# Optimization experiments

Hardware: AMD Instinct MI355X
Metric: run time of the kernel (lower is better)

The kernel has to match this reference:

```python
import jax, jax.numpy as jnp
import numpy as np

ANCHOR_PX = (32, 64, 96, 128)
FIELD = 16.0
POOL, TILES = 2, 3
TAU, NMS_IOU = 0.5, 0.3
MAX_DET = 512
HF, WF, DF = 128, 128, 512
HIDDEN = 1024


def _create_anchors():
    # anchors centered on the field grid, rows ordered (i, j, k): x,y = upper-left, w=h=size
    ii, jj, kk = np.meshgrid(np.arange(HF), np.arange(WF), np.arange(len(ANCHOR_PX)), indexing='ij')
    sz = np.asarray(ANCHOR_PX, np.float32)[kk]
    x = jj * FIELD + FIELD / 2 - sz / 2
    y = ii * FIELD + FIELD / 2 - sz / 2
    return np.stack([x.ravel(), y.ravel(), sz.ravel(), sz.ravel()], axis=1).astype(np.float32)


def setup_inputs() -> dict:
    key = jax.random.key(0)
    ks = jax.random.split(key, 8)
    return {
        'features': jax.random.normal(ks[0], (HF, WF, DF), jnp.float32),
        'rpn_obj': jax.random.normal(ks[1], (HF, WF, 2 * len(ANCHOR_PX)), jnp.float32),
        'rpn_reg': 0.1 * jax.random.normal(ks[2], (HF, WF, 4 * len(ANCHOR_PX)), jnp.float32),
        'anchors': jnp.asarray(_create_anchors()),
        'W1': 0.02 * jax.random.normal(ks[3], (TILES * TILES * DF, HIDDEN), jnp.float32),
        'b1': jnp.zeros((HIDDEN,), jnp.float32),
        'W2': 0.02 * jax.random.normal(ks[4], (HIDDEN, HIDDEN), jnp.float32),
        'b2': jnp.zeros((HIDDEN,), jnp.float32),
        'W3': 0.02 * jax.random.normal(ks[5], (HIDDEN, 4), jnp.float32),
        'b3': jnp.zeros((4,), jnp.float32),
    }


def _map_outputs(output, anchors):
    # faithful port of map_outputs: 3D RPN tensor -> per-anchor rows via gather
    K = len(ANCHOR_PX)
    ap = jnp.asarray(ANCHOR_PX, jnp.float32)
    idx = jnp.argmax(anchors[:, 3:4] == ap[None, :], axis=1).astype(jnp.int32)
    px = ((anchors[:, 0] + anchors[:, 2] / 2) / FIELD).astype(jnp.int32)
    py = ((anchors[:, 1] + anchors[:, 3] / 2) / FIELD).astype(jnp.int32)
    H, W, D = output.shape
    reshaped = output.reshape(H, W, K, D // K)
    return reshaped[py, px, idx]  # (Na, D//K)


def _unparameterize(reg, anchors):
    acx = anchors[:, 0] + anchors[:, 2] / 2
    acy = anchors[:, 1] + anchors[:, 3] / 2
    cx = acx + reg[:, 0] * anchors[:, 2]
    cy = acy + reg[:, 1] * anchors[:, 3]
    w = anchors[:, 2] * jnp.exp(reg[:, 2])
    h = anchors[:, 3] * jnp.exp(reg[:, 3])
    return jnp.stack([cx - w / 2, cy - h / 2, w, h], axis=1)


def _iou_matrix(boxes):
    x1, y1 = boxes[:, 0], boxes[:, 1]
    x2, y2 = x1 + boxes[:, 2], y1 + boxes[:, 3]
    ix = jnp.maximum(0.0, jnp.minimum(x2[:, None], x2[None, :]) - jnp.maximum(x1[:, None], x1[None, :]))
    iy = jnp.maximum(0.0, jnp.minimum(y2[:, None], y2[None, :]) - jnp.maximum(y1[:, None], y1[None, :]))
    inter = ix * iy
    area = boxes[:, 2] * boxes[:, 3]
    return inter / (area[:, None] + area[None, :] - inter + 1e-8)


def _nms_keep(iou, valid, thr):
    # greedy NMS on score-sorted boxes: sequential scan over rows
    n = valid.shape[0]
    rng = jnp.arange(n)
    def step(keep, i):
        suppressed = jnp.any((iou[i] > thr) & keep & (rng < i))
        k = valid[i] & jnp.logical_not(suppressed)
        return keep.at[i].set(k), k
    keep, _ = jax.lax.scan(step, jnp.zeros((n,), bool), rng)
    return keep


def _roialign(features, boxes):
    # pool x pool bilinear samples per tile, tiles x tiles tiles per box, max-pooled per tile
    M = boxes.shape[0]
    T = TILES * POOL
    t = (jnp.arange(T, dtype=jnp.float32) + 0.5) / T
    fx = (boxes[:, 0:1] + t[None, :] * boxes[:, 2:3]) / FIELD - 0.5  # (M, T)
    fy = (boxes[:, 1:2] + t[None, :] * boxes[:, 3:4]) / FIELD - 0.5
    def grid(c, n):
        c = jnp.clip(c, 0.0, n - 1.0)
        c0 = jnp.floor(c).astype(jnp.int32)
        c1 = jnp.minimum(c0 + 1, n - 1)
        return c0, c1, c - c0
    x0, x1, wx = grid(fx, WF)
    y0, y1, wy = grid(fy, HF)
    def g(yi, xi):
        return features[yi[:, :, None], xi[:, None, :]]  # (M, T, T, D)
    wy0, wy1 = (1 - wy)[:, :, None, None], wy[:, :, None, None]
    wx0, wx1 = (1 - wx)[:, None, :, None], wx[:, None, :, None]
    val = g(y0, x0) * wy0 * wx0 + g(y0, x1) * wy0 * wx1 + g(y1, x0) * wy1 * wx0 + g(y1, x1) * wy1 * wx1
    val = val.reshape(M, TILES, POOL, TILES, POOL, DF)
    return jnp.max(val, axis=(2, 4))  # (M, TILES, TILES, D)


def reference(features, rpn_obj, rpn_reg, anchors, W1, b1, W2, b2, W3, b3):
    obj = _map_outputs(rpn_obj, anchors)            # (Na, 2)
    reg = _map_outputs(rpn_reg, anchors)            # (Na, 4)
    scores = jax.nn.softmax(obj, axis=1)[:, 1]      # objectness
    boxes = _unparameterize(reg, anchors)           # proposals (Na, 4)
    # threshold + top-k (fixed-shape surrogate for boolean_mask)
    masked = jnp.where(scores > TAU, scores, -jnp.inf)
    top_scores, top_idx = jax.lax.top_k(masked, MAX_DET)
    valid = jnp.isfinite(top_scores)
    sel = boxes[top_idx]                            # (MAX_DET, 4)
    keep = _nms_keep(_iou_matrix(sel), valid, NMS_IOU)
    # roialign + fast-rcnn refinement head
    pooled = _roialign(features, sel).reshape(MAX_DET, -1)
    h = jax.nn.relu(pooled @ W1 + b1)
    h = jax.nn.relu(h @ W2 + b2)
    deltas = h @ W3 + b3
    refined = _unparameterize(deltas, sel)
    sc = jnp.where(valid, top_scores, 0.0)
    out = jnp.concatenate([refined, sc[:, None]], axis=1)
    return out * keep[:, None].astype(out.dtype)    # (MAX_DET, 5)
```

## Files before the change

kernel.cpp:

```cpp
#include <hip/hip_runtime.h>
#include <math.h>

#define HFD 128
#define WFD 128
#define DFD 512
#define KA  4
#define NA  (HFD*WFD*KA)
#define MAXD 512
#define HID 1024
#define FIN 4608
#define CMAX 2048
#define NBUCK 1025
#define BINCAP 64
#define TAUF 0.5f
#define NMS_THR 0.3f
#define SPLITK 8

typedef __bf16 bf16x8 __attribute__((ext_vector_type(8)));
typedef float  floatx4 __attribute__((ext_vector_type(4)));

__device__ __forceinline__ unsigned short f2bf(float x) {
    unsigned u = __float_as_uint(x);
    unsigned r = (u + 0x7FFFu + ((u >> 16) & 1u)) >> 16;
    return (unsigned short)r;
}

__global__ __launch_bounds__(256)
void front_kernel(const float* __restrict__ rpn_obj,
                  unsigned* __restrict__ hist,
                  unsigned long long* __restrict__ bins,
                  const float* __restrict__ W1,
                  unsigned short* __restrict__ W1t,
                  const float* __restrict__ W2,
                  unsigned short* __restrict__ W2t) {
    __shared__ float tile[32][33];
    int b = blockIdx.x;
    if (b < 256) {
        int n = b * 256 + threadIdx.x;
        float2 o = ((const float2*)rpn_obj)[n];
        float m  = fmaxf(o.x, o.y);
        float e0 = expf(o.x - m), e1 = expf(o.y - m);
        float s  = e1 / (e0 + e1);
        if (s > TAUF) {
            unsigned bits = __float_as_uint(s);
            unsigned bk = (bits - 0x3F000000u) >> 13;
            unsigned slot = atomicAdd(&hist[bk], 1u);
            if (slot < BINCAP)
                bins[bk * BINCAP + slot] =
                    ((unsigned long long)bits << 32) |
                    (unsigned long long)(~(unsigned)n);
        }
        return;
    }
    b -= 256;
    const float* W; unsigned short* Wt; int K, N;
    if (b < (FIN / 32) * (HID / 32)) { W = W1; Wt = W1t; K = FIN; N = HID; }
    else { b -= (FIN / 32) * (HID / 32); W = W2; Wt = W2t; K = HID; N = HID; }
    int bn = (b & (N / 32 - 1)) * 32;
    int bk = (b / (N / 32)) * 32;
    int tx = threadIdx.x & 31, ty = threadIdx.x >> 5;
#pragma unroll
    for (int r = 0; r < 32; r += 8)
        tile[ty + r][tx] = W[(long)(bk + ty + r) * N + bn + tx];
    __syncthreads();
#pragma unroll
    for (int r = 0; r < 32; r += 8)
        Wt[(long)(bn + ty + r) * K + bk + tx] = f2bf(tile[tx][ty + r]);
}

__global__ __launch_bounds__(1024)
void tgs_kernel(const unsigned* __restrict__ hist,
                const unsigned long long* __restrict__ bins,
                const float* __restrict__ rpn_reg,
                const float* __restrict__ anchors,
                float* __restrict__ sel,
                float* __restrict__ top_score,
                unsigned* __restrict__ valid_g) {
    __shared__ unsigned long long keys[CMAX];
    __shared__ unsigned Hs[NBUCK];
    __shared__ unsigned Ssc[1024];
    __shared__ unsigned cntS;
    __shared__ unsigned thrS;

    int tid = threadIdx.x;
    int wave = tid >> 6, lane = tid & 63;

    if (tid == 0) cntS = 0u;
    for (int i = tid; i < NBUCK; i += 1024) Hs[i] = hist[i];
    __syncthreads();
    unsigned sv = Hs[tid + 1];
    Ssc[tid] = sv;
    __syncthreads();
    for (int d = 1; d < 1024; d <<= 1) {
        unsigned add = (tid + d < 1024) ? Ssc[tid + d] : 0u;
        __syncthreads();
        Ssc[tid] += add;
        __syncthreads();
    }
    if (tid == 0 && Ssc[0] < MAXD) thrS = 0u;
    {
        unsigned Scur = Ssc[tid];
        unsigned Snxt = (tid == 1023) ? 0u : Ssc[tid + 1];
        if (Scur >= MAXD && Snxt < MAXD) thrS = (unsigned)(tid + 1);
    }
    __syncthreads();
    unsigned thr = thrS;

    for (int b = (int)thr + wave; b < NBUCK; b += 16) {
        unsigned c = Hs[b]; if (c > BINCAP) c = BINCAP;
        unsigned base = 0;
        if (lane == 0 && c > 0) base = atomicAdd(&cntS, c);
        base = __shfl(base, 0);
        if (c > 0 && lane < c && base + lane < CMAX)
            keys[base + lane] = bins[(long)b * BINCAP + lane];
    }
    __syncthreads();
    unsigned cnt = cntS; if (cnt > CMAX) cnt = CMAX;
    int SN = (cnt <= 1024) ? 1024 : CMAX;
    for (int i = tid; i < SN; i += 1024)
        if (i >= (int)cnt) keys[i] = 0ULL;
    __syncthreads();

    for (int k = 2; k <= SN; k <<= 1) {
        for (int j = k >> 1; j > 0; j >>= 1) {
            for (int i = tid; i < SN; i += 1024) {
                int ixj = i ^ j;
                if (ixj > i) {
                    unsigned long long a = keys[i], b = keys[ixj];
                    bool up = ((i & k) == 0);
                    if ((a < b) == up) { keys[i] = b; keys[ixj] = a; }
                }
            }
            __syncthreads();
        }
    }

    if (tid < MAXD) {
        unsigned long long e = keys[tid];
        unsigned sbits = (unsigned)(e >> 32);
        bool v = (sbits != 0u);
        unsigned idx = v ? (unsigned)(~(unsigned)e) : 0u;
        int cell = idx >> 2, kk = idx & 3;
        float4 rg = *(const float4*)&rpn_reg[cell * 16 + 4 * kk];
        float4 an = *(const float4*)&anchors[idx * 4];
        float acx = an.x + an.z * 0.5f;
        float acy = an.y + an.w * 0.5f;
        float cx = acx + rg.x * an.z;
        float cy = acy + rg.y * an.w;
        float w  = an.z * expf(rg.z);
        float h  = an.w * expf(rg.w);
        ((float4*)sel)[tid] = make_float4(cx - 0.5f * w, cy - 0.5f * h, w, h);
        top_score[tid] = v ? __uint_as_float(sbits) : 0.0f;
        valid_g[tid]   = v ? 1u : 0u;
    }
}

__global__ __launch_bounds__(512)
void iou_mask_kernel(const float* __restrict__ sel,
                     unsigned long long* __restrict__ mask) {
    int i = blockIdx.x;
    int j = threadIdx.x;
    float4 bi = ((const float4*)sel)[i];
    float4 bj = ((const float4*)sel)[j];
    float x2i = bi.x + bi.z, y2i = bi.y + bi.w;
    float x2j = bj.x + bj.z, y2j = bj.y + bj.w;
    float ai = bi.z * bi.w, aj = bj.z * bj.w;
    float ix = fmaxf(0.0f, fminf(x2i, x2j) - fmaxf(bi.x, bj.x));
    float iy = fmaxf(0.0f, fminf(y2i, y2j) - fmaxf(bi.y, bj.y));
    float inter = ix * iy;
    float iou = inter / (ai + aj - inter + 1e-8f);
    unsigned long long bal = __ballot(iou > NMS_THR);
    if ((j & 63) == 0) mask[i * 8 + (j >> 6)] = bal;
}

__global__ __launch_bounds__(64)
void nms_scan_kernel(const unsigned long long* __restrict__ mask,
                     const unsigned* __restrict__ valid,
                     unsigned* __restrict__ cidx,
                     unsigned* __restrict__ nkeep) {
    int lane = threadIdx.x;
    unsigned long long w[8][8];
#pragma unroll
    for (int g = 0; g < 8; ++g)
#pragma unroll
        for (int t = 0; t < 8; ++t)
            if (t <= g) w[g][t] = mask[(g * 64 + lane) * 8 + t];
    unsigned long long vb[8];
#pragma unroll
    for (int g = 0; g < 8; ++g)
        vb[g] = __ballot(valid[g * 64 + lane] != 0u);

    unsigned long long keepw[8];
#pragma unroll
    for (int g = 0; g < 8; ++g) {
        bool pre = false;
#pragma unroll
        for (int t = 0; t < 8; ++t)
            if (t < g) pre = pre || ((w[g][t] & keepw[t]) != 0ULL);
        unsigned long long alive = vb[g] & ~__ballot(pre);
        unsigned long long intra = w[g][g];
        unsigned long long kg = 0ULL;
        while (alive) {
            int b = __builtin_ctzll(alive);
            unsigned long long bit = 1ULL << b;
            kg |= bit;
            unsigned long long sup = __ballot((intra >> b) & 1ULL);
            alive &= ~(sup | bit);
        }
        keepw[g] = kg;
    }
    unsigned total = 0;
#pragma unroll
    for (int g = 0; g < 8; ++g) {
        unsigned long long kg = keepw[g];
        if ((kg >> lane) & 1ULL) {
            unsigned pos = total +
                (unsigned)__builtin_popcountll(kg & ((1ULL << lane) - 1ULL));
            cidx[pos] = (unsigned)(g * 64 + lane);
        }
        total += (unsigned)__builtin_popcountll(kg);
    }
    if (lane == 0) nkeep[0] = total;
}

__global__ __launch_bounds__(256)
void roialign_kernel(const float* __restrict__ feat,
                     const float* __restrict__ sel,
                     const unsigned* __restrict__ cidx,
                     const unsigned* __restrict__ nkeep,
                     unsigned short* __restrict__ pooled) {
    int m = blockIdx.x;
    if (m >= (int)nkeep[0]) return;
    int mrow = (int)cidx[m];
    int c = threadIdx.x;
    float4 b = ((const float4*)sel)[mrow];
    float bx = b.x, by = b.y, bw = b.z, bh = b.w;
    float vmax0[9], vmax1[9];
#pragma unroll
    for (int t = 0; t < 9; ++t) { vmax0[t] = -INFINITY; vmax1[t] = -INFINITY; }
#pragma unroll
    for (int p = 0; p < 6; ++p) {
        float fy = (by + ((float)p + 0.5f) / 6.0f * bh) / 16.0f - 0.5f;
        fy = fminf(fmaxf(fy, 0.0f), 127.0f);
        int y0 = (int)floorf(fy);
        int y1 = min(y0 + 1, 127);
        float wy = fy - (float)y0;
#pragma unroll
        for (int q = 0; q < 6; ++q) {
            float fx = (bx + ((float)q + 0.5f) / 6.0f * bw) / 16.0f - 0.5f;
            fx = fminf(fmaxf(fx, 0.0f), 127.0f);
            int x0 = (int)floorf(fx);
            int x1 = min(x0 + 1, 127);
            float wx = fx - (float)x0;
            const float* f00 = feat + (y0 * WFD + x0) * DFD;
            const float* f01 = feat + (y0 * WFD + x1) * DFD;
            const float* f10 = feat + (y1 * WFD + x0) * DFD;
            const float* f11 = feat + (y1 * WFD + x1) * DFD;
            float w00 = (1.0f - wy) * (1.0f - wx);
            float w01 = (1.0f - wy) * wx;
            float w10 = wy * (1.0f - wx);
            float w11 = wy * wx;
            int t = (p >> 1) * 3 + (q >> 1);
            float v0 = f00[c] * w00 + f01[c] * w01 + f10[c] * w10 + f11[c] * w11;
            float v1 = f00[c + 256] * w00 + f01[c + 256] * w01 +
                       f10[c + 256] * w10 + f11[c + 256] * w11;
            vmax0[t] = fmaxf(vmax0[t], v0);
            vmax1[t] = fmaxf(vmax1[t], v1);
        }
    }
#pragma unroll
    for (int t = 0; t < 9; ++t) {
        pooled[m * FIN + t * DFD + c] = f2bf(vmax0[t]);
        pooled[m * FIN + t * DFD + c + 256] = f2bf(vmax1[t]);
    }
}

#define LDSTRIDE 40
__global__ __launch_bounds__(256)
void mfma_gemm_kernel(const unsigned short* __restrict__ A,
                      const unsigned short* __restrict__ Bt,
                      float* __restrict__ Cpart,
                      const unsigned* __restrict__ nkeep,
                      int M, int N, int K) {
    int bm = blockIdx.y * 64;
    if (bm >= (int)nkeep[0]) return;
    __shared__ unsigned short As[64 * LDSTRIDE];
    __shared__ unsigned short Bs[64 * LDSTRIDE];
    int tid = threadIdx.x;
    int wave = tid >> 6, lane = tid & 63;
    int bn = blockIdx.x * 64;
    int KC = K / SPLITK;
    int ks = blockIdx.z * KC;

    floatx4 acc[4] = {};
    int lr = tid >> 2;
    int lk = (tid & 3) << 3;
    int frow = lane & 15, quad = lane >> 4;

    const unsigned short* Ap = A + (long)(bm + lr) * K + lk;
    const unsigned short* Bp = Bt + (long)(bn + lr) * K + lk;

    for (int k0 = ks; k0 < ks + KC; k0 += 32) {
        uint4 av = *(const uint4*)(Ap + k0);
        uint4 bv = *(const uint4*)(Bp + k0);
        *(uint4*)&As[lr * LDSTRIDE + lk] = av;
        *(uint4*)&Bs[lr * LDSTRIDE + lk] = bv;
        __syncthreads();
        bf16x8 af = *(const bf16x8*)&As[(wave * 16 + frow) * LDSTRIDE + quad * 8];
#pragma unroll
        for (int t = 0; t < 4; ++t) {
            bf16x8 bfv = *(const bf16x8*)&Bs[(t * 16 + frow) * LDSTRIDE + quad * 8];
            acc[t] = __builtin_amdgcn_mfma_f32_16x16x32_bf16(af, bfv, acc[t], 0, 0, 0);
        }
        __syncthreads();
    }

    float* Cp = Cpart + (long)blockIdx.z * M * N;
#pragma unroll
    for (int t = 0; t < 4; ++t) {
#pragma unroll
        for (int r = 0; r < 4; ++r) {
            int m = bm + wave * 16 + quad * 4 + r;
            int n = bn + t * 16 + frow;
            Cp[(long)m * N + n] = acc[t][r];
        }
    }
}

__global__ __launch_bounds__(256)
void reduce_bias_relu_kernel(const float* __restrict__ Cpart,
                             const float* __restrict__ bias,
                             unsigned short* __restrict__ out_bf,
                             const unsigned* __restrict__ nkeep,
                             int MN, int N) {
    int i4 = (blockIdx.x * blockDim.x + threadIdx.x) * 4;
    if (i4 >= MN) return;
    if ((unsigned)(i4 >> 10) >= nkeep[0]) return;
    float4 s = *(const float4*)&Cpart[i4];
#pragma unroll
    for (int z = 1; z < SPLITK; ++z) {
        float4 p = *(const float4*)&Cpart[(long)z * MN + i4];
        s.x += p.x; s.y += p.y; s.z += p.z; s.w += p.w;
    }
    int n = i4 & (N - 1);
    float4 bi = *(const float4*)&bias[n];
    s.x = fmaxf(s.x + bi.x, 0.0f);
    s.y = fmaxf(s.y + bi.y, 0.0f);
    s.z = fmaxf(s.z + bi.z, 0.0f);
    s.w = fmaxf(s.w + bi.w, 0.0f);
    uint2 o;
    o.x = (unsigned)f2bf(s.x) | ((unsigned)f2bf(s.y) << 16);
    o.y = (unsigned)f2bf(s.z) | ((unsigned)f2bf(s.w) << 16);
    *(uint2*)&out_bf[i4] = o;
}

__global__ __launch_bounds__(256)
void rowhead_kernel(const float* __restrict__ Cpart,
                    const float* __restrict__ b2,
                    const float* __restrict__ W3,
                    const float* __restrict__ b3,
                    const float* __restrict__ sel,
                    const float* __restrict__ top_score,
                    const unsigned* __restrict__ cidx,
                    const unsigned* __restrict__ nkeep,
                    float* __restrict__ out) {
    int p = blockIdx.x;
    if (p >= (int)nkeep[0]) return;
    __shared__ float red[4][4];
    int t = threadIdx.x;
    int wave = t >> 6, lane = t & 63;
    int c = t * 4;
    const int MN = MAXD * HID;
    float4 s = *(const float4*)&Cpart[(long)p * HID + c];
#pragma unroll
    for (int z = 1; z < SPLITK; ++z) {
        float4 q = *(const float4*)&Cpart[(long)z * MN + (long)p * HID + c];
        s.x += q.x; s.y += q.y; s.z += q.z; s.w += q.w;
    }
    float4 bi = *(const float4*)&b2[c];
    float h[4];
    h[0] = fmaxf(s.x + bi.x, 0.0f);
    h[1] = fmaxf(s.y + bi.y, 0.0f);
    h[2] = fmaxf(s.z + bi.z, 0.0f);
    h[3] = fmaxf(s.w + bi.w, 0.0f);
    float a0 = 0.f, a1 = 0.f, a2 = 0.f, a3 = 0.f;
#pragma unroll
    for (int i = 0; i < 4; ++i) {
        float4 w = *(const float4*)&W3[(c + i) * 4];
        a0 += h[i] * w.x; a1 += h[i] * w.y;
        a2 += h[i] * w.z; a3 += h[i] * w.w;
    }
#pragma unroll
    for (int off = 32; off > 0; off >>= 1) {
        a0 += __shfl_down(a0, off);
        a1 += __shfl_down(a1, off);
        a2 += __shfl_down(a2, off);
        a3 += __shfl_down(a3, off);
    }
    if (lane == 0) {
        red[wave][0] = a0; red[wave][1] = a1;
        red[wave][2] = a2; red[wave][3] = a3;
    }
    __syncthreads();
    if (t == 0) {
        int r = (int)cidx[p];
        float d0 = red[0][0] + red[1][0] + red[2][0] + red[3][0] + b3[0];
        float d1 = red[0][1] + red[1][1] + red[2][1] + red[3][1] + b3[1];
        float d2 = red[0][2] + red[1][2] + red[2][2] + red[3][2] + b3[2];
        float d3 = red[0][3] + red[1][3] + red[2][3] + red[3][3] + b3[3];
        float4 b = ((const float4*)sel)[r];
        float acx = b.x + 0.5f * b.z;
        float acy = b.y + 0.5f * b.w;
        float cx = acx + d0 * b.z;
        float cy = acy + d1 * b.w;
        float nw = b.z * expf(d2);
        float nh = b.w * expf(d3);
        out[r * 5 + 0] = cx - 0.5f * nw;
        out[r * 5 + 1] = cy - 0.5f * nh;
        out[r * 5 + 2] = nw;
        out[r * 5 + 3] = nh;
        out[r * 5 + 4] = top_score[r];
    }
}

extern "C" void kernel_launch(void* const* d_in, const int* in_sizes, int n_in,
                              void* d_out, int out_size, void* d_ws, size_t ws_size,
                              hipStream_t stream) {
    const float* features = (const float*)d_in[0];
    const float* rpn_obj  = (const float*)d_in[1];
    const float* rpn_reg  = (const float*)d_in[2];
    const float* anchors  = (const float*)d_in[3];
    const float* W1 = (const float*)d_in[4];
    const float* b1 = (const float*)d_in[5];
    const float* W2 = (const float*)d_in[6];
    const float* b2 = (const float*)d_in[7];
    const float* W3 = (const float*)d_in[8];
    const float* b3 = (const float*)d_in[9];
    float* out = (float*)d_out;

    char* ws = (char*)d_ws;
    size_t off = 0;
    auto alloc = [&](size_t bytes) {
        char* p = ws + off;
        off += (bytes + 255) & ~(size_t)255;
        return p;
    };
    unsigned* hist      = (unsigned*)alloc(NBUCK * sizeof(unsigned));
    unsigned long long* bins =
        (unsigned long long*)alloc((size_t)NBUCK * BINCAP * 8);
    float*    sel       = (float*)alloc(MAXD * 4 * sizeof(float));
    float*    top_score = (float*)alloc(MAXD * sizeof(float));
    unsigned* valid     = (unsigned*)alloc(MAXD * sizeof(unsigned));
    unsigned* cidx      = (unsigned*)alloc(MAXD * sizeof(unsigned));
    unsigned* nkeep     = (unsigned*)alloc(sizeof(unsigned));
    unsigned long long* mask = (unsigned long long*)alloc(MAXD * 8 * 8);
    unsigned short* pooled = (unsigned short*)alloc((size_t)MAXD * FIN * 2);
    unsigned short* W1t = (unsigned short*)alloc((size_t)FIN * HID * 2);
    unsigned short* W2t = (unsigned short*)alloc((size_t)HID * HID * 2);
    unsigned short* h1  = (unsigned short*)alloc((size_t)MAXD * HID * 2);
    float*    Cpart     = (float*)alloc((size_t)SPLITK * MAXD * HID * sizeof(float));
    (void)ws_size; (void)in_sizes; (void)n_in;

    hipMemsetAsync(hist, 0, NBUCK * sizeof(unsigned), stream);
    hipMemsetAsync(out, 0, (size_t)out_size * sizeof(float), stream);

    const int TBLOCKS = (FIN / 32) * (HID / 32) + (HID / 32) * (HID / 32);
    front_kernel<<<256 + TBLOCKS, 256, 0, stream>>>(rpn_obj, hist, bins,
                                                    W1, W1t, W2, W2t);
    tgs_kernel<<<1, 1024, 0, stream>>>(hist, bins, rpn_reg, anchors,
                                       sel, top_score, valid);
    iou_mask_kernel<<<MAXD, 512, 0, stream>>>(sel, mask);
    nms_scan_kernel<<<1, 64, 0, stream>>>(mask, valid, cidx, nkeep);
    roialign_kernel<<<MAXD, 256, 0, stream>>>(features, sel, cidx, nkeep,
                                              pooled);

    const int MN = MAXD * HID;
    mfma_gemm_kernel<<<dim3(HID / 64, MAXD / 64, SPLITK), 256, 0, stream>>>(
        pooled, W1t, Cpart, nkeep, MAXD, HID, FIN);
    reduce_bias_relu_kernel<<<MN / 4 / 256, 256, 0, stream>>>(
        Cpart, b1, h1, nkeep, MN, HID);
    mfma_gemm_kernel<<<dim3(HID / 64, MAXD / 64, SPLITK), 256, 0, stream>>>(
        h1, W2t, Cpart, nkeep, MAXD, HID, HID);
    rowhead_kernel<<<MAXD, 256, 0, stream>>>(Cpart, b2, W3, b3, sel,
                                             top_score, cidx, nkeep, out);
}
```

Before: 203.3 us.

## Fuse front pipeline stages into one cooperative persistent kernel with grid syncs

Merges the histogram, top-k sort, weight transpose, IoU mask, NMS scan and RoIAlign kernels (plus the hist memset) into a single 256-block cooperative kernel separated by grid.sync barriers. The goal is to remove several launch gaps and let the weight transpose run on the other blocks while block 0 does the serial top-k sort. The cost is that top-k now runs on one 256-thread block instead of 1024 threads. RoIAlign and transpose also spread over only 256 blocks with grid-wide barriers, so parallelism and latency hiding drop.

```diff
diff --git a/kernel.cpp b/kernel.cpp
--- a/kernel.cpp
+++ b/kernel.cpp
@@ -1,5 +1,8 @@
 #include <hip/hip_runtime.h>
+#include <hip/hip_cooperative_groups.h>
 #include <math.h>
+
+namespace cg = cooperative_groups;
 
 #define HFD 128
 #define WFD 128
@@ -15,6 +18,8 @@
 #define TAUF 0.5f
 #define NMS_THR 0.3f
 #define SPLITK 8
+#define TB_W1 ((FIN/32)*(HID/32))
+#define TB_ALL (TB_W1 + (HID/32)*(HID/32))
 
 typedef __bf16 bf16x8 __attribute__((ext_vector_type(8)));
 typedef float  floatx4 __attribute__((ext_vector_type(4)));
@@ -26,17 +31,39 @@
 }
 
 __global__ __launch_bounds__(256)
-void front_kernel(const float* __restrict__ rpn_obj,
-                  unsigned* __restrict__ hist,
-                  unsigned long long* __restrict__ bins,
-                  const float* __restrict__ W1,
-                  unsigned short* __restrict__ W1t,
-                  const float* __restrict__ W2,
-                  unsigned short* __restrict__ W2t) {
+void mega_kernel(const float* __restrict__ rpn_obj,
+                 const float* __restrict__ rpn_reg,
+                 const float* __restrict__ anchors,
+                 const float* __restrict__ features,
+                 const float* __restrict__ W1, unsigned short* __restrict__ W1t,
+                 const float* __restrict__ W2, unsigned short* __restrict__ W2t,
+                 unsigned* __restrict__ hist,
+                 unsigned long long* __restrict__ bins,
+                 float* __restrict__ sel,
+                 float* __restrict__ top_score,
+                 unsigned long long* __restrict__ mask,
+                 unsigned* __restrict__ cidx,
+                 unsigned* __restrict__ nkeep,
+                 unsigned short* __restrict__ pooled) {
+    cg::grid_group grid = cg::this_grid();
+    int b = blockIdx.x, tid = threadIdx.x;
+    int wave = tid >> 6, lane = tid & 63;
+
     __shared__ float tile[32][33];
-    int b = blockIdx.x;
-    if (b < 256) {
-        int n = b * 256 + threadIdx.x;
+    __shared__ unsigned long long keys[CMAX];
+    __shared__ unsigned Hs[NBUCK];
+    __shared__ unsigned Sp[256];
+    __shared__ float4 selS[MAXD];
+    __shared__ unsigned cntS, thrS;
+
+    {
+        int g = b * 256 + tid;
+        if (g < NBUCK) hist[g] = 0u;
+    }
+    grid.sync();
+
+    {
+        int n = b * 256 + tid;
         float2 o = ((const float2*)rpn_obj)[n];
         float m  = fmaxf(o.x, o.y);
         float e0 = expf(o.x - m), e1 = expf(o.y - m);
@@ -46,232 +73,227 @@
             unsigned bk = (bits - 0x3F000000u) >> 13;
             unsigned slot = atomicAdd(&hist[bk], 1u);
             if (slot < BINCAP)
-                bins[bk * BINCAP + slot] =
+                bins[(long)bk * BINCAP + slot] =
                     ((unsigned long long)bits << 32) |
                     (unsigned long long)(~(unsigned)n);
         }
-        return;
-    }
-    b -= 256;
-    const float* W; unsigned short* Wt; int K, N;
-    if (b < (FIN / 32) * (HID / 32)) { W = W1; Wt = W1t; K = FIN; N = HID; }
-    else { b -= (FIN / 32) * (HID / 32); W = W2; Wt = W2t; K = HID; N = HID; }
-    int bn = (b & (N / 32 - 1)) * 32;
-    int bk = (b / (N / 32)) * 32;
-    int tx = threadIdx.x & 31, ty = threadIdx.x >> 5;
-#pragma unroll
-    for (int r = 0; r < 32; r += 8)
-        tile[ty + r][tx] = W[(long)(bk + ty + r) * N + bn + tx];
+    }
+    __threadfence();
+    grid.sync();
+
+    if (b == 0) {
+        if (tid == 0) cntS = 0u;
+        for (int i = tid; i < NBUCK; i += 256) Hs[i] = hist[i];
+        __syncthreads();
+        unsigned s0 = Hs[4 * tid + 1], s1 = Hs[4 * tid + 2];
+        unsigned s2 = Hs[4 * tid + 3], s3 = Hs[4 * tid + 4];
+        Sp[tid] = s0 + s1 + s2 + s3;
+        __syncthreads();
+        for (int d = 1; d < 256; d <<= 1) {
+            unsigned add = (tid + d < 256) ? Sp[tid + d] : 0u;
+            __syncthreads();
+            Sp[tid] += add;
+            __syncthreads();
+        }
+        unsigned SpN = (tid < 255) ? Sp[tid + 1] : 0u;
+        __syncthreads();
+        unsigned suf3 = s3 + SpN;
+        unsigned suf2 = s2 + suf3;
+        unsigned suf1 = s1 + suf2;
+        unsigned suf0 = s0 + suf1;
+        if (tid == 0 && suf0 < MAXD) thrS = 0u;
+        {
+            unsigned su[5] = {suf0, suf1, suf2, suf3, SpN};
+#pragma unroll
+            for (int j = 0; j < 4; ++j)
+                if (su[j] >= MAXD && su[j + 1] < MAXD)
+                    thrS = (unsigned)(4 * tid + 1 + j);
+        }
+        __syncthreads();
+        unsigned thr = thrS;
+        for (int bk = (int)thr + wave; bk < NBUCK; bk += 4) {
+            unsigned c = Hs[bk]; if (c > BINCAP) c = BINCAP;
+            unsigned base = 0;
+            if (lane == 0 && c > 0) base = atomicAdd(&cntS, c);
+            base = __shfl(base, 0);
+            if (c > 0 && lane < c && base + lane < CMAX)
+                keys[base + lane] = bins[(long)bk * BINCAP + lane];
+        }
+        __syncthreads();
+        unsigned cnt = cntS; if (cnt > CMAX) cnt = CMAX;
+        int SN = (cnt <= 1024) ? 1024 : CMAX;
+        for (int i = tid; i < SN; i += 256)
+            if (i >= (int)cnt) keys[i] = 0ULL;
+        __syncthreads();
+        for (int k = 2; k <= SN; k <<= 1) {
+            for (int j = k >> 1; j > 0; j >>= 1) {
+                for (int i = tid; i < SN; i += 256) {
+                    int ixj = i ^ j;
+                    if (ixj > i) {
+                        unsigned long long a = keys[i], bb = keys[ixj];
+                        bool up = ((i & k) == 0);
+                        if ((a < bb) == up) { keys[i] = bb; keys[ixj] = a; }
+                    }
+                }
+                __syncthreads();
+            }
+        }
+        for (int r = tid; r < MAXD; r += 256) {
+            unsigned long long e = keys[r];
+            unsigned sbits = (unsigned)(e >> 32);
+            bool v = (sbits != 0u);
+            unsigned idx = v ? (unsigned)(~(unsigned)e) : 0u;
+            int cell = idx >> 2, kk = idx & 3;
+            float4 rg = *(const float4*)&rpn_reg[cell * 16 + 4 * kk];
+            float4 an = *(const float4*)&anchors[idx * 4];
+            float acx = an.x + an.z * 0.5f;
+            float acy = an.y + an.w * 0.5f;
+            float cx = acx + rg.x * an.z;
+            float cy = acy + rg.y * an.w;
+            float w  = an.z * expf(rg.z);
+            float h  = an.w * expf(rg.w);
+            ((float4*)sel)[r] = make_float4(cx - 0.5f * w, cy - 0.5f * h, w, h);
+            top_score[r] = v ? __uint_as_float(sbits) : 0.0f;
+        }
+    } else {
+        for (int tb = b - 1; tb < TB_ALL; tb += 255) {
+            const float* W; unsigned short* Wt; int K, N, t2 = tb;
+            if (t2 < TB_W1) { W = W1; Wt = W1t; K = FIN; N = HID; }
+            else { t2 -= TB_W1; W = W2; Wt = W2t; K = HID; N = HID; }
+            int bn = (t2 & (N / 32 - 1)) * 32;
+            int bk = (t2 / (N / 32)) * 32;
+            int tx = tid & 31, ty = tid >> 5;
+#pragma unroll
+            for (int r = 0; r < 32; r += 8)
+                tile[ty + r][tx] = W[(long)(bk + ty + r) * N + bn + tx];
+            __syncthreads();
+#pragma unroll
+            for (int r = 0; r < 32; r += 8)
+                Wt[(long)(bn + ty + r) * K + bk + tx] = f2bf(tile[tx][ty + r]);
+            __syncthreads();
+        }
+    }
+    __threadfence();
+    grid.sync();
+
+    for (int i = tid; i < MAXD; i += 256) selS[i] = ((const float4*)sel)[i];
     __syncthreads();
 #pragma unroll
-    for (int r = 0; r < 32; r += 8)
-        Wt[(long)(bn + ty + r) * K + bk + tx] = f2bf(tile[tx][ty + r]);
-}
-
-__global__ __launch_bounds__(1024)
-void tgs_kernel(const unsigned* __restrict__ hist,
-                const unsigned long long* __restrict__ bins,
-                const float* __restrict__ rpn_reg,
-                const float* __restrict__ anchors,
-                float* __restrict__ sel,
-                float* __restrict__ top_score,
-                unsigned* __restrict__ valid_g) {
-    __shared__ unsigned long long keys[CMAX];
-    __shared__ unsigned Hs[NBUCK];
-    __shared__ unsigned Ssc[1024];
-    __shared__ unsigned cntS;
-    __shared__ unsigned thrS;
-
-    int tid = threadIdx.x;
-    int wave = tid >> 6, lane = tid & 63;
-
-    if (tid == 0) cntS = 0u;
-    for (int i = tid; i < NBUCK; i += 1024) Hs[i] = hist[i];
-    __syncthreads();
-    unsigned sv = Hs[tid + 1];
-    Ssc[tid] = sv;
-    __syncthreads();
-    for (int d = 1; d < 1024; d <<= 1) {
-        unsigned add = (tid + d < 1024) ? Ssc[tid + d] : 0u;
-        __syncthreads();
-        Ssc[tid] += add;
-        __syncthreads();
-    }
-    if (tid == 0 && Ssc[0] < MAXD) thrS = 0u;
-    {
-        unsigned Scur = Ssc[tid];
-        unsigned Snxt = (tid == 1023) ? 0u : Ssc[tid + 1];
-        if (Scur >= MAXD && Snxt < MAXD) thrS = (unsigned)(tid + 1);
-    }
-    __syncthreads();
-    unsigned thr = thrS;
-
-    for (int b = (int)thr + wave; b < NBUCK; b += 16) {
-        unsigned c = Hs[b]; if (c > BINCAP) c = BINCAP;
-        unsigned base = 0;
-        if (lane == 0 && c > 0) base = atomicAdd(&cntS, c);
-        base = __shfl(base, 0);
-        if (c > 0 && lane < c && base + lane < CMAX)
-            keys[base + lane] = bins[(long)b * BINCAP + lane];
-    }
-    __syncthreads();
-    unsigned cnt = cntS; if (cnt > CMAX) cnt = CMAX;
-    int SN = (cnt <= 1024) ? 1024 : CMAX;
-    for (int i = tid; i < SN; i += 1024)
-        if (i >= (int)cnt) keys[i] = 0ULL;
-    __syncthreads();
-
-    for (int k = 2; k <= SN; k <<= 1) {
-        for (int j = k >> 1; j > 0; j >>= 1) {
-            for (int i = tid; i < SN; i += 1024) {
-                int ixj = i ^ j;
-                if (ixj > i) {
-                    unsigned long long a = keys[i], b = keys[ixj];
-                    bool up = ((i & k) == 0);
-                    if ((a < b) == up) { keys[i] = b; keys[ixj] = a; }
-                }
+    for (int rr = 0; rr < 2; ++rr) {
+        int i = 2 * b + rr;
+        float4 bi = selS[i];
+        float x2i = bi.x + bi.z, y2i = bi.y + bi.w;
+        float ai = bi.z * bi.w;
+#pragma unroll
+        for (int pass = 0; pass < 2; ++pass) {
+            int j = pass * 256 + tid;
+            float4 bj = selS[j];
+            float x2j = bj.x + bj.z, y2j = bj.y + bj.w;
+            float aj = bj.z * bj.w;
+            float ix = fmaxf(0.0f, fminf(x2i, x2j) - fmaxf(bi.x, bj.x));
+            float iy = fmaxf(0.0f, fminf(y2i, y2j) - fmaxf(bi.y, bj.y));
+            float inter = ix * iy;
+            float iou = inter / (ai + aj - inter + 1e-8f);
+            unsigned long long bal = __ballot(iou > NMS_THR);
+            if (lane == 0) mask[i * 8 + pass * 4 + wave] = bal;
+        }
+    }
+    __threadfence();
+    grid.sync();
+
+    if (b == 0 && wave == 0) {
+        unsigned long long w[8][8];
+#pragma unroll
+        for (int g = 0; g < 8; ++g)
+#pragma unroll
+            for (int t = 0; t < 8; ++t)
+                if (t <= g) w[g][t] = mask[(g * 64 + lane) * 8 + t];
+        unsigned long long vb[8];
+#pragma unroll
+        for (int g = 0; g < 8; ++g)
+            vb[g] = __ballot(top_score[g * 64 + lane] != 0.0f);
+        unsigned long long keepw[8];
+#pragma unroll
+        for (int g = 0; g < 8; ++g) {
+            bool pre = false;
+#pragma unroll
+            for (int t = 0; t < 8; ++t)
+                if (t < g) pre = pre || ((w[g][t] & keepw[t]) != 0ULL);
+            unsigned long long alive = vb[g] & ~__ballot(pre);
+            unsigned long long intra = w[g][g];
+            unsigned long long kg = 0ULL;
+            while (alive) {
+                int bb = __builtin_ctzll(alive);
+                unsigned long long bit = 1ULL << bb;
+                kg |= bit;
+                unsigned long long sup = __ballot((intra >> bb) & 1ULL);
+                alive &= ~(sup | bit);
             }
-            __syncthreads();
-        }
-    }
-
-    if (tid < MAXD) {
-        unsigned long long e = keys[tid];
-        unsigned sbits = (unsigned)(e >> 32);
-        bool v = (sbits != 0u);
-        unsigned idx = v ? (unsigned)(~(unsigned)e) : 0u;
-        int cell = idx >> 2, kk = idx & 3;
-        float4 rg = *(const float4*)&rpn_reg[cell * 16 + 4 * kk];
-        float4 an = *(const float4*)&anchors[idx * 4];
-        float acx = an.x + an.z * 0.5f;
-        float acy = an.y + an.w * 0.5f;
-        float cx = acx + rg.x * an.z;
-        float cy = acy + rg.y * an.w;
-        float w  = an.z * expf(rg.z);
-        float h  = an.w * expf(rg.w);
-        ((float4*)sel)[tid] = make_float4(cx - 0.5f * w, cy - 0.5f * h, w, h);
-        top_score[tid] = v ? __uint_as_float(sbits) : 0.0f;
-        valid_g[tid]   = v ? 1u : 0u;
-    }
-}
-
-__global__ __launch_bounds__(512)
-void iou_mask_kernel(const float* __restrict__ sel,
-                     unsigned long long* __restrict__ mask) {
-    int i = blockIdx.x;
-    int j = threadIdx.x;
-    float4 bi = ((const float4*)sel)[i];
-    float4 bj = ((const float4*)sel)[j];
-    float x2i = bi.x + bi.z, y2i = bi.y + bi.w;
-    float x2j = bj.x + bj.z, y2j = bj.y + bj.w;
-    float ai = bi.z * bi.w, aj = bj.z * bj.w;
-    float ix = fmaxf(0.0f, fminf(x2i, x2j) - fmaxf(bi.x, bj.x));
-    float iy = fmaxf(0.0f, fminf(y2i, y2j) - fmaxf(bi.y, bj.y));
-    float inter = ix * iy;
-    float iou = inter / (ai + aj - inter + 1e-8f);
-    unsigned long long bal = __ballot(iou > NMS_THR);
-    if ((j & 63) == 0) mask[i * 8 + (j >> 6)] = bal;
-}
-
-__global__ __launch_bounds__(64)
-void nms_scan_kernel(const unsigned long long* __restrict__ mask,
-                     const unsigned* __restrict__ valid,
-                     unsigned* __restrict__ cidx,
-                     unsigned* __restrict__ nkeep) {
-    int lane = threadIdx.x;
-    unsigned long long w[8][8];
-#pragma unroll
-    for (int g = 0; g < 8; ++g)
-#pragma unroll
-        for (int t = 0; t < 8; ++t)
-            if (t <= g) w[g][t] = mask[(g * 64 + lane) * 8 + t];
-    unsigned long long vb[8];
-#pragma unroll
-    for (int g = 0; g < 8; ++g)
-        vb[g] = __ballot(valid[g * 64 + lane] != 0u);
-
-    unsigned long long keepw[8];
-#pragma unroll
-    for (int g = 0; g < 8; ++g) {
-        bool pre = false;
-#pragma unroll
-        for (int t = 0; t < 8; ++t)
-            if (t < g) pre = pre || ((w[g][t] & keepw[t]) != 0ULL);
-        unsigned long long alive = vb[g] & ~__ballot(pre);
-        unsigned long long intra = w[g][g];
-        unsigned long long kg = 0ULL;
-        while (alive) {
-            int b = __builtin_ctzll(alive);
-            unsigned long long bit = 1ULL << b;
-            kg |= bit;
-            unsigned long long sup = __ballot((intra >> b) & 1ULL);
-            alive &= ~(sup | bit);
-        }
-        keepw[g] = kg;
-    }
-    unsigned total = 0;
-#pragma unroll
-    for (int g = 0; g < 8; ++g) {
-        unsigned long long kg = keepw[g];
-        if ((kg >> lane) & 1ULL) {
-            unsigned pos = total +
-                (unsigned)__builtin_popcountll(kg & ((1ULL << lane) - 1ULL));
-            cidx[pos] = (unsigned)(g * 64 + lane);
-        }
-        total += (unsigned)__builtin_popcountll(kg);
-    }
-    if (lane == 0) nkeep[0] = total;
-}
-
-__global__ __launch_bounds__(256)
-void roialign_kernel(const float* __restrict__ feat,
-                     const float* __restrict__ sel,
-                     const unsigned* __restrict__ cidx,
-                     const unsigned* __restrict__ nkeep,
-                     unsigned short* __restrict__ pooled) {
-    int m = blockIdx.x;
-    if (m >= (int)nkeep[0]) return;
-    int mrow = (int)cidx[m];
-    int c = threadIdx.x;
-    float4 b = ((const float4*)sel)[mrow];
-    float bx = b.x, by = b.y, bw = b.z, bh = b.w;
-    float vmax0[9], vmax1[9];
-#pragma unroll
-    for (int t = 0; t < 9; ++t) { vmax0[t] = -INFINITY; vmax1[t] = -INFINITY; }
-#pragma unroll
-    for (int p = 0; p < 6; ++p) {
-        float fy = (by + ((float)p + 0.5f) / 6.0f * bh) / 16.0f - 0.5f;
-        fy = fminf(fmaxf(fy, 0.0f), 127.0f);
-        int y0 = (int)floorf(fy);
-        int y1 = min(y0 + 1, 127);
-        float wy = fy - (float)y0;
-#pragma unroll
-        for (int q = 0; q < 6; ++q) {
-            float fx = (bx + ((float)q + 0.5f) / 6.0f * bw) / 16.0f - 0.5f;
-            fx = fminf(fmaxf(fx, 0.0f), 127.0f);
-            int x0 = (int)floorf(fx);
-            int x1 = min(x0 + 1, 127);
-            float wx = fx - (float)x0;
-            const float* f00 = feat + (y0 * WFD + x0) * DFD;
-            const float* f01 = feat + (y0 * WFD + x1) * DFD;
-            const float* f10 = feat + (y1 * WFD + x0) * DFD;
-            const float* f11 = feat + (y1 * WFD + x1) * DFD;
-            float w00 = (1.0f - wy) * (1.0f - wx);
-            float w01 = (1.0f - wy) * wx;
-            float w10 = wy * (1.0f - wx);
-            float w11 = wy * wx;
-            int t = (p >> 1) * 3 + (q >> 1);
-            float v0 = f00[c] * w00 + f01[c] * w01 + f10[c] * w10 + f11[c] * w11;
-            float v1 = f00[c + 256] * w00 + f01[c + 256] * w01 +
-                       f10[c + 256] * w10 + f11[c + 256] * w11;
-            vmax0[t] = fmaxf(vmax0[t], v0);
-            vmax1[t] = fmaxf(vmax1[t], v1);
-        }
-    }
-#pragma unroll
-    for (int t = 0; t < 9; ++t) {
-        pooled[m * FIN + t * DFD + c] = f2bf(vmax0[t]);
-        pooled[m * FIN + t * DFD + c + 256] = f2bf(vmax1[t]);
+            keepw[g] = kg;
+        }
+        unsigned total = 0;
+#pragma unroll
+        for (int g = 0; g < 8; ++g) {
+            unsigned long long kg = keepw[g];
+            if ((kg >> lane) & 1ULL) {
+                unsigned pos = total +
+                    (unsigned)__builtin_popcountll(kg & ((1ULL << lane) - 1ULL));
+                cidx[pos] = (unsigned)(g * 64 + lane);
+            }
+            total += (unsigned)__builtin_popcountll(kg);
+        }
+        if (lane == 0) nkeep[0] = total;
+        __threadfence();
+    }
+    grid.sync();
+
+    unsigned P = nkeep[0];
+    int c = tid;
+#pragma unroll
+    for (int rr = 0; rr < 2; ++rr) {
+        int m = 2 * b + rr;
+        if (m >= (int)P) continue;
+        int mrow = (int)cidx[m];
+        float4 bx4 = selS[mrow];
+        float bx = bx4.x, by = bx4.y, bw = bx4.z, bh = bx4.w;
+        float vmax0[9], vmax1[9];
+#pragma unroll
+        for (int t = 0; t < 9; ++t) { vmax0[t] = -INFINITY; vmax1[t] = -INFINITY; }
+#pragma unroll
+        for (int p = 0; p < 6; ++p) {
+            float fy = (by + ((float)p + 0.5f) / 6.0f * bh) / 16.0f - 0.5f;
+            fy = fminf(fmaxf(fy, 0.0f), 127.0f);
+            int y0 = (int)floorf(fy);
+            int y1 = min(y0 + 1, 127);
+            float wy = fy - (float)y0;
+#pragma unroll
+            for (int q = 0; q < 6; ++q) {
+                float fx = (bx + ((float)q + 0.5f) / 6.0f * bw) / 16.0f - 0.5f;
+                fx = fminf(fmaxf(fx, 0.0f), 127.0f);
+                int x0 = (int)floorf(fx);
+                int x1 = min(x0 + 1, 127);
+                float wx = fx - (float)x0;
+                const float* f00 = features + (y0 * WFD + x0) * DFD;
+                const float* f01 = features + (y0 * WFD + x1) * DFD;
+                const float* f10 = features + (y1 * WFD + x0) * DFD;
+                const float* f11 = features + (y1 * WFD + x1) * DFD;
+                float w00 = (1.0f - wy) * (1.0f - wx);
+                float w01 = (1.0f - wy) * wx;
+                float w10 = wy * (1.0f - wx);
+                float w11 = wy * wx;
+                int t = (p >> 1) * 3 + (q >> 1);
+                float v0 = f00[c] * w00 + f01[c] * w01 + f10[c] * w10 + f11[c] * w11;
+                float v1 = f00[c + 256] * w00 + f01[c + 256] * w01 +
+                           f10[c + 256] * w10 + f11[c + 256] * w11;
+                vmax0[t] = fmaxf(vmax0[t], v0);
+                vmax1[t] = fmaxf(vmax1[t], v1);
+            }
+        }
+#pragma unroll
+        for (int t = 0; t < 9; ++t) {
+            pooled[m * FIN + t * DFD + c] = f2bf(vmax0[t]);
+            pooled[m * FIN + t * DFD + c + 256] = f2bf(vmax1[t]);
+        }
     }
 }
 
@@ -450,7 +472,6 @@
         (unsigned long long*)alloc((size_t)NBUCK * BINCAP * 8);
     float*    sel       = (float*)alloc(MAXD * 4 * sizeof(float));
     float*    top_score = (float*)alloc(MAXD * sizeof(float));
-    unsigned* valid     = (unsigned*)alloc(MAXD * sizeof(unsigned));
     unsigned* cidx      = (unsigned*)alloc(MAXD * sizeof(unsigned));
     unsigned* nkeep     = (unsigned*)alloc(sizeof(unsigned));
     unsigned long long* mask = (unsigned long long*)alloc(MAXD * 8 * 8);
@@ -461,18 +482,16 @@
     float*    Cpart     = (float*)alloc((size_t)SPLITK * MAXD * HID * sizeof(float));
     (void)ws_size; (void)in_sizes; (void)n_in;
 
-    hipMemsetAsync(hist, 0, NBUCK * sizeof(unsigned), stream);
     hipMemsetAsync(out, 0, (size_t)out_size * sizeof(float), stream);
 
-    const int TBLOCKS = (FIN / 32) * (HID / 32) + (HID / 32) * (HID / 32);
-    front_kernel<<<256 + TBLOCKS, 256, 0, stream>>>(rpn_obj, hist, bins,
-                                                    W1, W1t, W2, W2t);
-    tgs_kernel<<<1, 1024, 0, stream>>>(hist, bins, rpn_reg, anchors,
-                                       sel, top_score, valid);
-    iou_mask_kernel<<<MAXD, 512, 0, stream>>>(sel, mask);
-    nms_scan_kernel<<<1, 64, 0, stream>>>(mask, valid, cidx, nkeep);
-    roialign_kernel<<<MAXD, 256, 0, stream>>>(features, sel, cidx, nkeep,
-                                              pooled);
+    void* args[] = {
+        (void*)&rpn_obj, (void*)&rpn_reg, (void*)&anchors, (void*)&features,
+        (void*)&W1, (void*)&W1t, (void*)&W2, (void*)&W2t,
+        (void*)&hist, (void*)&bins, (void*)&sel, (void*)&top_score,
+        (void*)&mask, (void*)&cidx, (void*)&nkeep, (void*)&pooled
+    };
+    hipLaunchCooperativeKernel((const void*)mega_kernel, dim3(256), dim3(256),
+                               args, 0, stream);
 
     const int MN = MAXD * HID;
     mfma_gemm_kernel<<<dim3(HID / 64, MAXD / 64, SPLITK), 256, 0, stream>>>(
```

Result: slower. 422.1 us (+107.6%).
